# Performance work log

Hardware: AMD Instinct MI355X
Metric: run time of the kernel (lower is better)

Reference implementation:

```python
import jax, jax.numpy as jnp
import numpy as np
import math

N = 100000
E = 1600000
D_IN = 128
H = 128
OUT = 10
NEG = -1e30


def setup_inputs() -> dict:
    key = jax.random.key(0)
    ks = jax.random.split(key, 24)
    def lin(k, fi, fo):
        s = 1.0 / np.sqrt(fi)
        return jax.random.uniform(k, (fi, fo), jnp.float32, -s, s)
    inp = {
        'x': jax.random.normal(ks[0], (N, D_IN), jnp.float32),
        'edge_index': jax.random.randint(ks[1], (2, E), 0, N, jnp.int64),
        'W1': lin(ks[2], D_IN, H), 'b1': jnp.zeros((H,), jnp.float32),
        'ws1': lin(ks[3], H, 1), 'bs1': jnp.zeros((1,), jnp.float32),
        'W2': lin(ks[4], H, H), 'b2': jnp.zeros((H,), jnp.float32),
        'ws2': lin(ks[5], H, 1), 'bs2': jnp.zeros((1,), jnp.float32),
        'W3': lin(ks[6], H, H), 'b3': jnp.zeros((H,), jnp.float32),
        'ws3': lin(ks[7], H, 1), 'bs3': jnp.zeros((1,), jnp.float32),
        'M1': lin(ks[8], 2 * H, H), 'bm1': jnp.zeros((H,), jnp.float32),
        'M2': lin(ks[9], H, H // 2), 'bm2': jnp.zeros((H // 2,), jnp.float32),
        'M3': lin(ks[10], H // 2, OUT), 'bm3': jnp.zeros((OUT,), jnp.float32),
    }
    return inp


def _gcn(x, W, b, src, dst, node_mask, edge_mask):
    # GCNConv with self-loops: deg[i] = self_loop + in_degree over valid edges
    deg = node_mask + jax.ops.segment_sum(edge_mask, dst, num_segments=N)
    dinv = jnp.where(deg > 0, jax.lax.rsqrt(deg), 0.0)
    coef = edge_mask * dinv[src] * dinv[dst]            # [E]
    agg = jax.ops.segment_sum(coef[:, None] * x[src], dst, num_segments=N)
    agg = agg + (node_mask * dinv * dinv)[:, None] * x   # self-loop term
    return (agg @ W + b) * node_mask[:, None]


def _sag_pool(x, ws, bs, src, dst, node_mask, edge_mask, k):
    # score via 1-dim GCNConv, top-k (ratio 0.5) select, tanh gating, edge filtering
    score = _gcn(x, ws, bs, src, dst, node_mask, edge_mask)[:, 0]
    _, idx = jax.lax.top_k(jnp.where(node_mask > 0, score, -jnp.inf), k)
    new_mask = jnp.zeros((N,), x.dtype).at[idx].set(1.0)
    x_new = x * jnp.tanh(score)[:, None] * new_mask[:, None]
    e_new = edge_mask * new_mask[src] * new_mask[dst]
    return x_new, new_mask, e_new


def _readout(x, mask, k):
    mean = jnp.sum(x * mask[:, None], axis=0) / k
    mx = jnp.max(jnp.where(mask[:, None] > 0, x, NEG), axis=0)
    return jnp.concatenate([mean, mx])[None, :]   # [1, 2H]


def reference(x, edge_index, W1, b1, ws1, bs1, W2, b2, ws2, bs2, W3, b3, ws3, bs3, M1, bm1, M2, bm2, M3, bm3):
    src, dst = edge_index[0], edge_index[1]
    nm0 = jnp.ones((N,), jnp.float32)
    em0 = jnp.ones((E,), jnp.float32)
    k1 = math.ceil(0.5 * N)
    k2 = math.ceil(0.5 * k1)
    k3 = math.ceil(0.5 * k2)

    h1 = jax.nn.relu(_gcn(x, W1, b1, src, dst, nm0, em0))
    x1, nm1, em1 = _sag_pool(h1, ws1, bs1, src, dst, nm0, em0, k1)
    r1 = _readout(x1, nm1, k1)

    h2 = jax.nn.relu(_gcn(x1, W2, b2, src, dst, nm1, em1))
    x2, nm2, em2 = _sag_pool(h2, ws2, bs2, src, dst, nm1, em1, k2)
    r2 = _readout(x2, nm2, k2)

    h3 = jax.nn.relu(_gcn(x2, W3, b3, src, dst, nm2, em2))
    x3, nm3, em3 = _sag_pool(h3, ws3, bs3, src, dst, nm2, em2, k3)
    r3 = _readout(x3, nm3, k3)

    readout = r1 + r2 + r3                              # [1, 2H]
    y = jax.nn.relu(readout @ M1 + bm1)
    y = jax.nn.relu(y @ M2 + bm2)
    y = y @ M3 + bm3
    return jax.nn.log_softmax(y, axis=1)
```

## Files before the change

### kernel.cpp

```cpp
#include <hip/hip_runtime.h>
#include <cstdint>
#include <cstddef>

#define NN 100000
#define EE 1600000
#define HH 128
#define NB_N 391
#define NBKT 391
#define CAP 5120


static __device__ __forceinline__ unsigned fsort_(float f){
  unsigned u = __float_as_uint(f);
  return (u & 0x80000000u) ? ~u : (u | 0x80000000u);
}
static __device__ __forceinline__ unsigned bfbits_(float f){
  unsigned u = __float_as_uint(f);
  return (u + 0x7FFFu + ((u >> 16) & 1u)) >> 16;
}
static __device__ __forceinline__ unsigned bfpack_(float f0, float f1){
  return bfbits_(f0) | (bfbits_(f1) << 16);
}
static __device__ __forceinline__ float bflo_(unsigned u){ return __uint_as_float(u << 16); }
static __device__ __forceinline__ float bfhi_(unsigned u){ return __uint_as_float(u & 0xFFFF0000u); }

__global__ void k_edgeflag(const int* __restrict__ ei, unsigned* __restrict__ state,
                           unsigned* __restrict__ bktcnt){
  int t = threadIdx.x;
  if(t < 64){
    int v = ei[2*t + 1];
    unsigned long long m = __ballot(v != 0);
    if(t == 0) state[8] = (m == 0ull) ? 1u : 0u;
  }
  if(t >= 12 && t < 24) state[t] = 0u;
  for(int j=t; j<NBKT; j+=256) bktcnt[j] = 0u;
}

__global__ __launch_bounds__(256) void k_binA(const int* __restrict__ ei,
                     const unsigned* __restrict__ state,
                     unsigned* __restrict__ bktcnt, unsigned* __restrict__ staging){
  __shared__ unsigned lcnt[NBKT];
  __shared__ unsigned lloc[NBKT];
  int t = threadIdx.x;
  for(int j=t; j<NBKT; j+=256){ lcnt[j] = 0u; lloc[j] = 0u; }
  bool i64 = (state[8] != 0u);
  int e0 = blockIdx.x*4096;
  int es[16], ed[16];
  #pragma unroll
  for(int k=0;k<16;k++){
    int e = e0 + k*256 + t;
    int s = -1, d = 0;
    if(e < EE){
      if(i64){ s = ei[2*e]; d = ei[2*EE + 2*e]; }
      else   { s = ei[e];   d = ei[EE + e]; }
    }
    es[k] = s; ed[k] = d;
  }
  __syncthreads();
  #pragma unroll
  for(int k=0;k<16;k++){
    if(es[k] >= 0) atomicAdd(&lcnt[ed[k]>>8], 1u);
  }
  __syncthreads();
  for(int j=t; j<NBKT; j+=256){
    unsigned c = lcnt[j];
    lcnt[j] = c ? atomicAdd(&bktcnt[j], c) : 0u;
  }
  __syncthreads();
  #pragma unroll
  for(int k=0;k<16;k++){
    if(es[k] >= 0){
      int b = ed[k] >> 8;
      unsigned off = lcnt[b] + atomicAdd(&lloc[b], 1u);
      if(off < CAP)
        staging[(unsigned)b*CAP + off] = (unsigned)es[k] | (((unsigned)(ed[k] & 255)) << 17);
    }
  }
}

__global__ __launch_bounds__(256) void k_binB(const unsigned* __restrict__ staging,
                     const unsigned* __restrict__ bktcnt,
                     int* __restrict__ rs, int* __restrict__ rl, int* __restrict__ col,
                     float* __restrict__ dinv){
  __shared__ unsigned hist[256];
  __shared__ unsigned pref[256];
  __shared__ unsigned lfill[256];
  __shared__ unsigned baseSh;
  int t = threadIdx.x;
  int b = blockIdx.x;
  unsigned s = 0;
  for(int j=t; j<b; j+=256) s += bktcnt[j];
  pref[t] = s;
  __syncthreads();
  for(int off=128; off>0; off>>=1){
    if(t < off) pref[t] += pref[t+off];
    __syncthreads();
  }
  if(t == 0) baseSh = pref[0];
  __syncthreads();
  unsigned base = baseSh;
  unsigned cnt = bktcnt[b]; if(cnt > CAP) cnt = CAP;
  hist[t] = 0u; lfill[t] = 0u;
  __syncthreads();
  const unsigned* st = staging + (unsigned)b*CAP;
  for(unsigned i=t; i<cnt; i+=256) atomicAdd(&hist[st[i]>>17], 1u);
  __syncthreads();
  unsigned h = hist[t];
  pref[t] = h;
  __syncthreads();
  for(int off=1; off<256; off<<=1){
    unsigned u = (t >= off) ? pref[t-off] : 0u;
    __syncthreads();
    pref[t] += u;
    __syncthreads();
  }
  unsigned excl = pref[t] - h;
  int node = b*256 + t;
  if(node < NN){
    rs[node] = (int)(base + excl);
    rl[node] = (int)h;
    dinv[node] = rsqrtf(1.f + (float)h);
  }
  __syncthreads();
  pref[t] = excl;
  __syncthreads();
  for(unsigned i=t; i<cnt; i+=256){
    unsigned w = st[i];
    unsigned dl = w >> 17;
    unsigned pos = base + pref[dl] + atomicAdd(&lfill[dl], 1u);
    col[pos] = (int)(w & 0x1FFFFu);
  }
}

template<int MODE>
__global__ __launch_bounds__(256) void k_gemm(const void* __restrict__ xin_,
        const float* __restrict__ gate, const int* __restrict__ alist, int nrows,
        const float* __restrict__ W, unsigned short* __restrict__ y16){
  __shared__ float sX[16][68];
  __shared__ float sW[16][64];
  __shared__ int rowid[64];
  __shared__ float rowg[64];
  int row0 = blockIdx.x*64, col0 = blockIdx.y*64;
  int t = threadIdx.x;
  if(t < 64){
    int gr = row0 + t;
    int node = -1; float gg = 0.f;
    if(gr < nrows){
      node = MODE ? alist[gr] : gr;
      gg = MODE ? gate[node] : 1.f;
    }
    rowid[t] = node; rowg[t] = gg;
  }
  __syncthreads();
  int tx = t & 15, ty = t >> 4;
  float acc[4][4] = {{0.f}};
  const float* xf = (const float*)xin_;
  const unsigned short* xh = (const unsigned short*)xin_;
  for(int kb=0; kb<HH; kb+=16){
    #pragma unroll
    for(int j=0;j<4;j++){
      int r = (t>>4) + j*16;
      int k = t & 15;
      int node = rowid[r];
      float v = 0.f;
      if(node >= 0){
        if(MODE) v = __uint_as_float(((unsigned)xh[(size_t)node*HH + kb + k]) << 16) * rowg[r];
        else     v = xf[(size_t)node*HH + kb + k];
      }
      sX[k][r] = v;
    }
    #pragma unroll
    for(int j=0;j<4;j++){
      int k = (t>>6) + j*4;
      int c = t & 63;
      sW[k][c] = W[(size_t)(kb+k)*HH + col0 + c];
    }
    __syncthreads();
    #pragma unroll
    for(int k=0;k<16;k++){
      float4 xv = *(const float4*)&sX[k][ty*4];
      float4 wv = *(const float4*)&sW[k][tx*4];
      float xs[4] = {xv.x, xv.y, xv.z, xv.w};
      float wsv[4] = {wv.x, wv.y, wv.z, wv.w};
      #pragma unroll
      for(int a=0;a<4;a++)
        #pragma unroll
        for(int b=0;b<4;b++)
          acc[a][b] += xs[a]*wsv[b];
    }
    __syncthreads();
  }
  #pragma unroll
  for(int a=0;a<4;a++){
    int node = rowid[ty*4 + a];
    if(node >= 0){
      uint2 o;
      o.x = bfpack_(acc[a][0], acc[a][1]);
      o.y = bfpack_(acc[a][2], acc[a][3]);
      *(uint2*)&y16[(size_t)node*HH + col0 + tx*4] = o;
    }
  }
}

template<int LIST>
__global__ __launch_bounds__(256) void k_agg(const unsigned short* __restrict__ y16,
        const float* __restrict__ dinv,
        const int* __restrict__ rs, const int* __restrict__ rl,
        const int* __restrict__ col, const int* __restrict__ alist,
        const float* __restrict__ bias, const float* __restrict__ wsc,
        unsigned short* __restrict__ h16, float* __restrict__ p,
        unsigned* __restrict__ hist){
  if(blockIdx.x < 512) hist[blockIdx.x*256 + threadIdx.x] = 0u;
  int w = (blockIdx.x*256 + threadIdx.x) >> 6;
  int lane = threadIdx.x & 63;
  int g = lane >> 4, c = lane & 15;
  int node = LIST ? alist[w] : w;
  float di = dinv[node];
  int e0 = rs[node], len = rl[node];
  float a0=0,a1=0,a2=0,a3=0,a4=0,a5=0,a6=0,a7=0;
  int i = g;
  for(; i + 4 < len; i += 8){
    int s0 = col[e0+i], s1 = col[e0+i+4];
    float d0 = dinv[s0], d1 = dinv[s1];
    uint4 v0 = ((const uint4*)(y16 + (size_t)s0*HH))[c];
    uint4 v1 = ((const uint4*)(y16 + (size_t)s1*HH))[c];
    a0 += d0*bflo_(v0.x) + d1*bflo_(v1.x);
    a1 += d0*bfhi_(v0.x) + d1*bfhi_(v1.x);
    a2 += d0*bflo_(v0.y) + d1*bflo_(v1.y);
    a3 += d0*bfhi_(v0.y) + d1*bfhi_(v1.y);
    a4 += d0*bflo_(v0.z) + d1*bflo_(v1.z);
    a5 += d0*bfhi_(v0.z) + d1*bfhi_(v1.z);
    a6 += d0*bflo_(v0.w) + d1*bflo_(v1.w);
    a7 += d0*bfhi_(v0.w) + d1*bfhi_(v1.w);
  }
  if(i < len){
    int s = col[e0+i];
    float ds = dinv[s];
    uint4 v = ((const uint4*)(y16 + (size_t)s*HH))[c];
    a0 += ds*bflo_(v.x); a1 += ds*bfhi_(v.x);
    a2 += ds*bflo_(v.y); a3 += ds*bfhi_(v.y);
    a4 += ds*bflo_(v.z); a5 += ds*bfhi_(v.z);
    a6 += ds*bflo_(v.w); a7 += ds*bfhi_(v.w);
  }
  a0 += __shfl_xor(a0,16,64); a0 += __shfl_xor(a0,32,64);
  a1 += __shfl_xor(a1,16,64); a1 += __shfl_xor(a1,32,64);
  a2 += __shfl_xor(a2,16,64); a2 += __shfl_xor(a2,32,64);
  a3 += __shfl_xor(a3,16,64); a3 += __shfl_xor(a3,32,64);
  a4 += __shfl_xor(a4,16,64); a4 += __shfl_xor(a4,32,64);
  a5 += __shfl_xor(a5,16,64); a5 += __shfl_xor(a5,32,64);
  a6 += __shfl_xor(a6,16,64); a6 += __shfl_xor(a6,32,64);
  a7 += __shfl_xor(a7,16,64); a7 += __shfl_xor(a7,32,64);
  uint4 sv = ((const uint4*)(y16 + (size_t)node*HH))[c];
  const float4* b4 = (const float4*)bias;
  float4 bb0 = b4[2*c], bb1 = b4[2*c+1];
  float d2 = di*di;
  float o0 = fmaxf(di*a0 + d2*bflo_(sv.x) + bb0.x, 0.f);
  float o1 = fmaxf(di*a1 + d2*bfhi_(sv.x) + bb0.y, 0.f);
  float o2 = fmaxf(di*a2 + d2*bflo_(sv.y) + bb0.z, 0.f);
  float o3 = fmaxf(di*a3 + d2*bfhi_(sv.y) + bb0.w, 0.f);
  float o4 = fmaxf(di*a4 + d2*bflo_(sv.z) + bb1.x, 0.f);
  float o5 = fmaxf(di*a5 + d2*bfhi_(sv.z) + bb1.y, 0.f);
  float o6 = fmaxf(di*a6 + d2*bflo_(sv.w) + bb1.z, 0.f);
  float o7 = fmaxf(di*a7 + d2*bfhi_(sv.w) + bb1.w, 0.f);
  if(g == 0){
    uint4 o;
    o.x = bfpack_(o0,o1); o.y = bfpack_(o2,o3);
    o.z = bfpack_(o4,o5); o.w = bfpack_(o6,o7);
    ((uint4*)(h16 + (size_t)node*HH))[c] = o;
  }
  const float4* w4 = (const float4*)wsc;
  float4 w0 = w4[2*c], w1 = w4[2*c+1];
  float pp = o0*w0.x + o1*w0.y + o2*w0.z + o3*w0.w
           + o4*w1.x + o5*w1.y + o6*w1.z + o7*w1.w;
  pp += __shfl_xor(pp, 1, 64);
  pp += __shfl_xor(pp, 2, 64);
  pp += __shfl_xor(pp, 4, 64);
  pp += __shfl_xor(pp, 8, 64);
  if(lane == 0) p[node] = pp;
}

template<int LIST>
__global__ void k_score(const float* __restrict__ p, const float* __restrict__ dinv,
                        const int* __restrict__ rs, const int* __restrict__ rl,
                        const int* __restrict__ col, const int* __restrict__ alist, int n,
                        const float* __restrict__ bs, float* __restrict__ score,
                        unsigned* __restrict__ key, unsigned* __restrict__ hist){
  int w = blockIdx.x*256 + threadIdx.x;
  if(w >= n) return;
  int i = LIST ? alist[w] : w;
  float di = dinv[i];
  float s = 0.f;
  int e0 = rs[i], len = rl[i];
  for(int e=e0; e<e0+len; e++){
    int cidx = col[e];
    s += dinv[cidx]*p[cidx];
  }
  float sc = di*s + di*di*p[i] + bs[0];
  score[i] = sc;
  unsigned kv = fsort_(sc);
  key[i] = kv;
  atomicAdd(&hist[kv>>16], 1u);
}

__global__ void k_hist_lo(const unsigned* __restrict__ key, const unsigned* __restrict__ state,
                          unsigned* __restrict__ histB){
  int i = blockIdx.x*256 + threadIdx.x;
  if(i < NN){
    unsigned kv = key[i];
    if((kv >> 16) == state[0]) atomicAdd(&histB[kv & 0xFFFFu], 1u);
  }
}
__global__ void k_pick(const unsigned* __restrict__ hist, unsigned* __restrict__ state,
                       int k_in, int mode){
  __shared__ unsigned csum[256];
  int t = threadIdx.x;
  const uint4* h4 = (const uint4*)(hist + t*256);
  unsigned s = 0;
  for(int j=0;j<64;j++){ uint4 v = h4[j]; s += v.x+v.y+v.z+v.w; }
  csum[t] = s;
  __syncthreads();
  for(int off=1; off<256; off<<=1){
    unsigned v = (t+off < 256) ? csum[t+off] : 0u;
    __syncthreads();
    csum[t] += v;
    __syncthreads();
  }
  unsigned k = (mode == 0) ? (unsigned)k_in : state[1];
  unsigned above = csum[t] - s;
  if(above < k && above + s >= k){
    unsigned run = above;
    for(int j=255; j>=0; j--){
      unsigned c = hist[t*256+j];
      if(run + c >= k){
        if(mode == 0){ state[0] = (unsigned)(t*256+j); state[1] = k - run; }
        else { state[2] = (state[0] << 16) | (unsigned)(t*256+j); state[3] = k - run; }
        break;
      }
      run += c;
    }
  }
}

__global__ __launch_bounds__(256) void k_maskCR(unsigned* __restrict__ key,
        const float* __restrict__ score, const unsigned* __restrict__ state,
        const unsigned short* __restrict__ h16,
        unsigned char* __restrict__ selm, float* __restrict__ gate,
        int* __restrict__ alist_out, unsigned* __restrict__ acounter,
        float* __restrict__ rpart, int slotbase){
  __shared__ int wcnt[4];
  __shared__ int priorSh;
  __shared__ int redi[256];
  __shared__ float gl[256];
  __shared__ unsigned char slf[256];
  __shared__ float4 red[256];
  __shared__ float out2[256];
  int t = threadIdx.x;
  int i = blockIdx.x*256 + t;
  unsigned T = state[2];
  int trem = (int)state[3];
  unsigned kv = (i < NN) ? key[i] : 0u;
  bool match = (kv == T);
  unsigned long long m = __ballot(match);
  int lane = t & 63, wid = t >> 6;
  if(lane == 0) wcnt[wid] = __popcll(m);
  if(t == 0) priorSh = 0;
  __syncthreads();
  int hasMatch = wcnt[0] | wcnt[1] | wcnt[2] | wcnt[3];
  int bbase = blockIdx.x*256;
  if(hasMatch){
    int cm = 0;
    for(int j = t*4; j < bbase; j += 1024){
      uint4 kk = *(const uint4*)&key[j];
      cm += (kk.x==T) + (kk.y==T) + (kk.z==T) + (kk.w==T);
    }
    redi[t] = cm;
    __syncthreads();
    for(int off=128; off>0; off>>=1){
      if(t < off) redi[t] += redi[t+off];
      __syncthreads();
    }
    if(t == 0) priorSh = redi[0];
    __syncthreads();
  }
  int pre = 0;
  for(int w=0; w<wid; w++) pre += wcnt[w];
  int lrank = __popcll(m & ((1ull << lane) - 1ull));
  int rank = priorSh + pre + lrank;
  bool sel = (kv > T) || (match && rank < trem);
  float gg = sel ? tanhf(score[i]) : 0.f;
  gl[t] = gg;
  slf[t] = sel ? 1 : 0;
  if(i < NN){
    selm[i] = sel ? 1 : 0;
    gate[i] = gg;
    if(!sel) key[i] = 0u;
  }
  unsigned long long sm = __ballot(sel);
  unsigned abase = 0;
  if(lane == 0) abase = atomicAdd(acounter, (unsigned)__popcll(sm));
  abase = (unsigned)__shfl((int)abase, 0, 64);
  if(sel) alist_out[abase + __popcll(sm & ((1ull << lane) - 1ull))] = i;
  __syncthreads();
  int ch = t & 15;
  int slot = t >> 4;
  float mm[8] = {0,0,0,0,0,0,0,0};
  float MM[8] = {-1e30f,-1e30f,-1e30f,-1e30f,-1e30f,-1e30f,-1e30f,-1e30f};
  for(int itr=0; itr<16; itr++){
    int nl = slot + itr*16;
    int node = bbase + nl;
    if(node < NN && slf[nl]){
      float g = gl[nl];
      uint4 v = ((const uint4*)(h16 + (size_t)node*HH))[ch];
      float x0 = g*bflo_(v.x), x1 = g*bfhi_(v.x);
      float x2 = g*bflo_(v.y), x3 = g*bfhi_(v.y);
      float x4 = g*bflo_(v.z), x5 = g*bfhi_(v.z);
      float x6 = g*bflo_(v.w), x7 = g*bfhi_(v.w);
      mm[0]+=x0; mm[1]+=x1; mm[2]+=x2; mm[3]+=x3;
      mm[4]+=x4; mm[5]+=x5; mm[6]+=x6; mm[7]+=x7;
      MM[0]=fmaxf(MM[0],x0); MM[1]=fmaxf(MM[1],x1); MM[2]=fmaxf(MM[2],x2); MM[3]=fmaxf(MM[3],x3);
      MM[4]=fmaxf(MM[4],x4); MM[5]=fmaxf(MM[5],x5); MM[6]=fmaxf(MM[6],x6); MM[7]=fmaxf(MM[7],x7);
    }
  }
  #pragma unroll
  for(int half=0; half<2; half++){
    red[t] = make_float4(mm[half*4+0],mm[half*4+1],mm[half*4+2],mm[half*4+3]);
    __syncthreads();
    if(t < 16){
      float4 sacc = red[t];
      for(int j=1;j<16;j++){
        float4 o = red[t + 16*j];
        sacc.x += o.x; sacc.y += o.y; sacc.z += o.z; sacc.w += o.w;
      }
      int d = t*8 + half*4;
      out2[d+0] = sacc.x; out2[d+1] = sacc.y; out2[d+2] = sacc.z; out2[d+3] = sacc.w;
    }
    __syncthreads();
    red[t] = make_float4(MM[half*4+0],MM[half*4+1],MM[half*4+2],MM[half*4+3]);
    __syncthreads();
    if(t < 16){
      float4 sacc = red[t];
      for(int j=1;j<16;j++){
        float4 o = red[t + 16*j];
        sacc.x = fmaxf(sacc.x,o.x); sacc.y = fmaxf(sacc.y,o.y);
        sacc.z = fmaxf(sacc.z,o.z); sacc.w = fmaxf(sacc.w,o.w);
      }
      int d = 128 + t*8 + half*4;
      out2[d+0] = sacc.x; out2[d+1] = sacc.y; out2[d+2] = sacc.z; out2[d+3] = sacc.w;
    }
    __syncthreads();
  }
  rpart[(size_t)(slotbase + blockIdx.x)*256 + t] = out2[t];
}

__global__ __launch_bounds__(256) void k_compact(const int* __restrict__ alist, int n,
        const unsigned char* __restrict__ selm,
        const int* __restrict__ rs_old, const int* __restrict__ rl_old,
        const int* __restrict__ col_old,
        int* __restrict__ rs_new, int* __restrict__ rl_new, int* __restrict__ col_new,
        float* __restrict__ dinv, unsigned* __restrict__ ecnt){
  __shared__ unsigned gcnt[16];
  __shared__ unsigned gbase[16];
  __shared__ unsigned blkbase;
  int t = threadIdx.x;
  int g = t >> 4, lane = t & 15;
  int gsh = ((t >> 4) & 3) * 16;
  int idx = blockIdx.x*16 + g;
  int node = -1, e0 = 0, len = 0;
  if(idx < n){ node = alist[idx]; e0 = rs_old[node]; len = rl_old[node]; }
  int cnt = 0;
  for(int i=lane; i<len; i+=16) cnt += selm[col_old[e0+i]];
  cnt += __shfl_xor(cnt,1,64); cnt += __shfl_xor(cnt,2,64);
  cnt += __shfl_xor(cnt,4,64); cnt += __shfl_xor(cnt,8,64);
  if(lane == 0) gcnt[g] = (node >= 0) ? (unsigned)cnt : 0u;
  __syncthreads();
  if(t == 0){
    unsigned s = 0;
    for(int j=0;j<16;j++){ gbase[j] = s; s += gcnt[j]; }
    blkbase = s ? atomicAdd(ecnt, s) : 0u;
  }
  __syncthreads();
  unsigned base = blkbase + gbase[g];
  if(node >= 0 && lane == 0){
    rs_new[node] = (int)base;
    rl_new[node] = cnt;
    dinv[node] = rsqrtf(1.f + (float)cnt);
  }
  int pos = (int)base;
  for(int i0=0; i0<len; i0+=16){
    int i = i0 + lane;
    bool keep = false; int s = 0;
    if(i < len){ s = col_old[e0+i]; keep = (selm[s] != 0); }
    unsigned long long b = __ballot(keep);
    unsigned gb = (unsigned)((b >> gsh) & 0xFFFFull);
    int rank = __popc(gb & ((1u << lane) - 1u));
    if(keep) col_new[pos + rank] = s;
    pos += __popc(gb);
  }
}

__global__ void k_mlp(const float* __restrict__ rpart,
                      const float* __restrict__ M1, const float* __restrict__ bm1,
                      const float* __restrict__ M2, const float* __restrict__ bm2,
                      const float* __restrict__ M3, const float* __restrict__ bm3,
                      float* __restrict__ out){
  __shared__ float R[256];
  __shared__ float y1[128];
  __shared__ float y2[64];
  __shared__ float y3[16];
  int t = threadIdx.x;
  const float kinv[3] = {1.f/50000.f, 1.f/25000.f, 1.f/12500.f};
  if(t < 128){
    float acc = 0.f;
    for(int l=0; l<3; l++){
      float s0=0.f,s1=0.f,s2=0.f,s3=0.f;
      int base = l*NB_N;
      int j = 0;
      for(; j+3 < NB_N; j += 4){
        s0 += rpart[(size_t)(base+j  )*256 + t];
        s1 += rpart[(size_t)(base+j+1)*256 + t];
        s2 += rpart[(size_t)(base+j+2)*256 + t];
        s3 += rpart[(size_t)(base+j+3)*256 + t];
      }
      for(; j < NB_N; j++) s0 += rpart[(size_t)(base+j)*256 + t];
      acc += ((s0+s1)+(s2+s3)) * kinv[l];
    }
    R[t] = acc;
  } else {
    float acc = 0.f;
    for(int l=0; l<3; l++){
      float m0=-1e30f,m1=-1e30f,m2=-1e30f,m3=-1e30f;
      int base = l*NB_N;
      int j = 0;
      for(; j+3 < NB_N; j += 4){
        m0 = fmaxf(m0, rpart[(size_t)(base+j  )*256 + t]);
        m1 = fmaxf(m1, rpart[(size_t)(base+j+1)*256 + t]);
        m2 = fmaxf(m2, rpart[(size_t)(base+j+2)*256 + t]);
        m3 = fmaxf(m3, rpart[(size_t)(base+j+3)*256 + t]);
      }
      for(; j < NB_N; j++) m0 = fmaxf(m0, rpart[(size_t)(base+j)*256 + t]);
      acc += fmaxf(fmaxf(m0,m1), fmaxf(m2,m3));
    }
    R[t] = acc;
  }
  __syncthreads();
  if(t < 128){
    float a = bm1[t];
    for(int d=0; d<256; d++) a += R[d]*M1[d*128+t];
    y1[t] = fmaxf(a, 0.f);
  }
  __syncthreads();
  if(t < 64){
    float a = bm2[t];
    for(int d=0; d<128; d++) a += y1[d]*M2[d*64+t];
    y2[t] = fmaxf(a, 0.f);
  }
  __syncthreads();
  if(t < 10){
    float a = bm3[t];
    for(int d=0; d<64; d++) a += y2[d]*M3[d*10+t];
    y3[t] = a;
  }
  __syncthreads();
  if(t == 0){
    float mx = -1e30f;
    for(int o=0;o<10;o++) mx = fmaxf(mx, y3[o]);
    float s = 0.f;
    for(int o=0;o<10;o++) s += expf(y3[o]-mx);
    float ls = logf(s);
    for(int o=0;o<10;o++) out[o] = y3[o] - mx - ls;
  }
}

extern "C" void kernel_launch(void* const* d_in, const int* in_sizes, int n_in,
                              void* d_out, int out_size, void* d_ws, size_t ws_size,
                              hipStream_t stream){
  (void)in_sizes; (void)n_in; (void)out_size; (void)ws_size;
  const float* x  = (const float*)d_in[0];
  const int*   ei = (const int*)d_in[1];
  const float* W[3]   = {(const float*)d_in[2],  (const float*)d_in[6],  (const float*)d_in[10]};
  const float* bb[3]  = {(const float*)d_in[3],  (const float*)d_in[7],  (const float*)d_in[11]};
  const float* wsc[3] = {(const float*)d_in[4],  (const float*)d_in[8],  (const float*)d_in[12]};
  const float* bsc[3] = {(const float*)d_in[5],  (const float*)d_in[9],  (const float*)d_in[13]};
  const float* M1  = (const float*)d_in[14];
  const float* bm1 = (const float*)d_in[15];
  const float* M2  = (const float*)d_in[16];
  const float* bm2 = (const float*)d_in[17];
  const float* M3  = (const float*)d_in[18];
  const float* bm3 = (const float*)d_in[19];
  float* out = (float*)d_out;

  char* base = (char*)d_ws;
  size_t off = 0;
  auto alloc = [&](size_t bytes)->char*{
    char* ptr = base + off;
    off += (bytes + 511) & ~(size_t)511;
    return ptr;
  };
  unsigned short* y16  = (unsigned short*)alloc((size_t)NN*HH*2);
  unsigned short* h16  = (unsigned short*)alloc((size_t)NN*HH*2);
  int*      col0      = (int*)     alloc((size_t)EE*4);
  int*      col1      = (int*)     alloc((size_t)EE*4);
  int*      col2      = (int*)     alloc((size_t)EE*4);
  unsigned* staging   = (unsigned*)alloc((size_t)NBKT*CAP*4);
  int*      rs0       = (int*)     alloc((size_t)NN*4);
  int*      rl0       = (int*)     alloc((size_t)NN*4);
  int*      rs1       = (int*)     alloc((size_t)NN*4);
  int*      rl1       = (int*)     alloc((size_t)NN*4);
  int*      rs2       = (int*)     alloc((size_t)NN*4);
  int*      rl2       = (int*)     alloc((size_t)NN*4);
  float*    dinv      = (float*)   alloc((size_t)NN*4);
  float*    pbuf      = (float*)   alloc((size_t)NN*4);
  float*    score     = (float*)   alloc((size_t)NN*4);
  float*    gate      = (float*)   alloc((size_t)NN*4);
  unsigned* key       = (unsigned*)alloc((size_t)NN*4);
  unsigned char* selm = (unsigned char*)alloc((size_t)NN);
  int*      alistA    = (int*)     alloc((size_t)50000*4);
  int*      alistB    = (int*)     alloc((size_t)25000*4);
  unsigned* hist      = (unsigned*)alloc((size_t)2*65536*4);
  unsigned* bktcnt    = (unsigned*)alloc((size_t)(NBKT+1)*4);
  unsigned* state     = (unsigned*)alloc(256);
  float*    rpart     = (float*)   alloc((size_t)3*NB_N*256*4);

  k_edgeflag<<<1,256,0,stream>>>(ei, state, bktcnt);
  k_binA<<<NBKT,256,0,stream>>>(ei, state, bktcnt, staging);
  k_binB<<<NBKT,256,0,stream>>>(staging, bktcnt, rs0, rl0, col0, dinv);

  k_gemm<0><<<dim3(1563,2),256,0,stream>>>(x, nullptr, nullptr, NN, W[0], y16);
  k_agg<0><<<25000,256,0,stream>>>(y16, dinv, rs0, rl0, col0, nullptr, bb[0], wsc[0], h16, pbuf, hist);
  k_score<0><<<NB_N,256,0,stream>>>(pbuf, dinv, rs0, rl0, col0, nullptr, NN, bsc[0], score, key, hist);
  k_pick<<<1,256,0,stream>>>(hist, state, 50000, 0);
  k_hist_lo<<<NB_N,256,0,stream>>>(key, state, hist + 65536);
  k_pick<<<1,256,0,stream>>>(hist + 65536, state, 0, 1);
  k_maskCR<<<NB_N,256,0,stream>>>(key, score, state, h16, selm, gate, alistA, state+12, rpart, 0);
  k_compact<<<3125,256,0,stream>>>(alistA, 50000, selm, rs0, rl0, col0, rs1, rl1, col1, dinv, state+16);

  k_gemm<1><<<dim3(782,2),256,0,stream>>>(h16, gate, alistA, 50000, W[1], y16);
  k_agg<1><<<12500,256,0,stream>>>(y16, dinv, rs1, rl1, col1, alistA, bb[1], wsc[1], h16, pbuf, hist);
  k_score<1><<<196,256,0,stream>>>(pbuf, dinv, rs1, rl1, col1, alistA, 50000, bsc[1], score, key, hist);
  k_pick<<<1,256,0,stream>>>(hist, state, 25000, 0);
  k_hist_lo<<<NB_N,256,0,stream>>>(key, state, hist + 65536);
  k_pick<<<1,256,0,stream>>>(hist + 65536, state, 0, 1);
  k_maskCR<<<NB_N,256,0,stream>>>(key, score, state, h16, selm, gate, alistB, state+13, rpart, NB_N);
  k_compact<<<1563,256,0,stream>>>(alistB, 25000, selm, rs1, rl1, col1, rs2, rl2, col2, dinv, state+17);

  k_gemm<1><<<dim3(391,2),256,0,stream>>>(h16, gate, alistB, 25000, W[2], y16);
  k_agg<1><<<6250,256,0,stream>>>(y16, dinv, rs2, rl2, col2, alistB, bb[2], wsc[2], h16, pbuf, hist);
  k_score<1><<<98,256,0,stream>>>(pbuf, dinv, rs2, rl2, col2, alistB, 25000, bsc[2], score, key, hist);
  k_pick<<<1,256,0,stream>>>(hist, state, 12500, 0);
  k_hist_lo<<<NB_N,256,0,stream>>>(key, state, hist + 65536);
  k_pick<<<1,256,0,stream>>>(hist + 65536, state, 0, 1);
  k_maskCR<<<NB_N,256,0,stream>>>(key, score, state, h16, selm, gate, alistA, state+14, rpart, 2*NB_N);

  k_mlp<<<1,256,0,stream>>>(rpart, M1, bm1, M2, bm2, M3, bm3, out);
}
```

Before: 802.9 us.

## Fuse CSR build and top-k select stages into persistent kernels with grid barriers

Merges the edge-flag, bin-A and bin-B CSR construction kernels into one persistent 256-block kernel separated by software grid barriers. It also fuses the pick, low-histogram, mask/readout and edge-compaction kernels of each pooling stage into a single k_select kernel, with every block redundantly computing the histogram pick. The aim is to cut many small kernel launches and their serialization gaps. In exchange it depends on all 256 blocks being co-resident for the spin barrier, and the fused phases run with fewer blocks than the separate kernels did.

```diff
diff --git a/kernel.cpp b/kernel.cpp
--- a/kernel.cpp
+++ b/kernel.cpp
@@ -8,6 +8,7 @@
 #define NB_N 391
 #define NBKT 391
 #define CAP 5120
+#define GSEL 256
 
 
 static __device__ __forceinline__ unsigned fsort_(float f){
@@ -24,111 +25,159 @@
 static __device__ __forceinline__ float bflo_(unsigned u){ return __uint_as_float(u << 16); }
 static __device__ __forceinline__ float bfhi_(unsigned u){ return __uint_as_float(u & 0xFFFF0000u); }
 
-__global__ void k_edgeflag(const int* __restrict__ ei, unsigned* __restrict__ state,
-                           unsigned* __restrict__ bktcnt){
+static __device__ __forceinline__ void gridbar(unsigned* bar, unsigned nblk){
+  __syncthreads();
+  if(threadIdx.x == 0){
+    __threadfence();
+    unsigned g = __hip_atomic_load(&bar[1], __ATOMIC_RELAXED, __HIP_MEMORY_SCOPE_AGENT);
+    unsigned old = __hip_atomic_fetch_add(&bar[0], 1u, __ATOMIC_ACQ_REL, __HIP_MEMORY_SCOPE_AGENT);
+    if(old == nblk - 1u){
+      __hip_atomic_store(&bar[0], 0u, __ATOMIC_RELAXED, __HIP_MEMORY_SCOPE_AGENT);
+      __hip_atomic_store(&bar[1], g + 1u, __ATOMIC_RELEASE, __HIP_MEMORY_SCOPE_AGENT);
+    } else {
+      unsigned cur;
+      do {
+        __builtin_amdgcn_s_sleep(2);
+        cur = __hip_atomic_load(&bar[1], __ATOMIC_ACQUIRE, __HIP_MEMORY_SCOPE_AGENT);
+      } while(cur == g);
+    }
+    __threadfence();
+  }
+  __syncthreads();
+}
+
+static __device__ void pick_blk(const unsigned* __restrict__ hist, unsigned k,
+                                unsigned* csum, unsigned* outB, unsigned* outR){
+  __syncthreads();
   int t = threadIdx.x;
+  const uint4* h4 = (const uint4*)(hist + t*256);
+  unsigned s = 0;
+  for(int j=0;j<64;j++){ uint4 v = h4[j]; s += v.x+v.y+v.z+v.w; }
+  csum[t] = s;
+  __syncthreads();
+  for(int off=1; off<256; off<<=1){
+    unsigned v = (t+off < 256) ? csum[t+off] : 0u;
+    __syncthreads();
+    csum[t] += v;
+    __syncthreads();
+  }
+  unsigned above = csum[t] - s;
+  if(above < k && above + s >= k){
+    unsigned run = above;
+    for(int j=255; j>=0; j--){
+      unsigned c = hist[t*256+j];
+      if(run + c >= k){ *outB = (unsigned)(t*256+j); *outR = k - run; break; }
+      run += c;
+    }
+  }
+  __syncthreads();
+}
+
+__global__ __launch_bounds__(256) void k_csr(const int* __restrict__ ei,
+        unsigned* __restrict__ bktcnt, unsigned* __restrict__ staging,
+        int* __restrict__ rs, int* __restrict__ rl, int* __restrict__ col,
+        float* __restrict__ dinv, unsigned* __restrict__ state, unsigned* __restrict__ bar){
+  __shared__ unsigned lcnt[NBKT];
+  __shared__ unsigned lloc[NBKT];
+  __shared__ unsigned histo[256];
+  __shared__ unsigned pref[256];
+  __shared__ unsigned lfill[256];
+  __shared__ unsigned baseSh;
+  __shared__ int i64f;
+  int t = threadIdx.x;
+  int b = blockIdx.x;
+  int G = gridDim.x;
+  for(int j = b*256 + t; j < NBKT; j += G*256) bktcnt[j] = 0u;
+  if(b == 0 && t >= 12 && t < 24) state[t] = 0u;
   if(t < 64){
     int v = ei[2*t + 1];
     unsigned long long m = __ballot(v != 0);
-    if(t == 0) state[8] = (m == 0ull) ? 1u : 0u;
-  }
-  if(t >= 12 && t < 24) state[t] = 0u;
-  for(int j=t; j<NBKT; j+=256) bktcnt[j] = 0u;
-}
-
-__global__ __launch_bounds__(256) void k_binA(const int* __restrict__ ei,
-                     const unsigned* __restrict__ state,
-                     unsigned* __restrict__ bktcnt, unsigned* __restrict__ staging){
-  __shared__ unsigned lcnt[NBKT];
-  __shared__ unsigned lloc[NBKT];
-  int t = threadIdx.x;
-  for(int j=t; j<NBKT; j+=256){ lcnt[j] = 0u; lloc[j] = 0u; }
-  bool i64 = (state[8] != 0u);
-  int e0 = blockIdx.x*4096;
-  int es[16], ed[16];
-  #pragma unroll
-  for(int k=0;k<16;k++){
-    int e = e0 + k*256 + t;
-    int s = -1, d = 0;
-    if(e < EE){
-      if(i64){ s = ei[2*e]; d = ei[2*EE + 2*e]; }
-      else   { s = ei[e];   d = ei[EE + e]; }
-    }
-    es[k] = s; ed[k] = d;
-  }
-  __syncthreads();
-  #pragma unroll
-  for(int k=0;k<16;k++){
-    if(es[k] >= 0) atomicAdd(&lcnt[ed[k]>>8], 1u);
-  }
-  __syncthreads();
-  for(int j=t; j<NBKT; j+=256){
-    unsigned c = lcnt[j];
-    lcnt[j] = c ? atomicAdd(&bktcnt[j], c) : 0u;
-  }
-  __syncthreads();
-  #pragma unroll
-  for(int k=0;k<16;k++){
-    if(es[k] >= 0){
-      int b = ed[k] >> 8;
-      unsigned off = lcnt[b] + atomicAdd(&lloc[b], 1u);
-      if(off < CAP)
-        staging[(unsigned)b*CAP + off] = (unsigned)es[k] | (((unsigned)(ed[k] & 255)) << 17);
-    }
-  }
-}
-
-__global__ __launch_bounds__(256) void k_binB(const unsigned* __restrict__ staging,
-                     const unsigned* __restrict__ bktcnt,
-                     int* __restrict__ rs, int* __restrict__ rl, int* __restrict__ col,
-                     float* __restrict__ dinv){
-  __shared__ unsigned hist[256];
-  __shared__ unsigned pref[256];
-  __shared__ unsigned lfill[256];
-  __shared__ unsigned baseSh;
-  int t = threadIdx.x;
-  int b = blockIdx.x;
-  unsigned s = 0;
-  for(int j=t; j<b; j+=256) s += bktcnt[j];
-  pref[t] = s;
-  __syncthreads();
-  for(int off=128; off>0; off>>=1){
-    if(t < off) pref[t] += pref[t+off];
-    __syncthreads();
-  }
-  if(t == 0) baseSh = pref[0];
-  __syncthreads();
-  unsigned base = baseSh;
-  unsigned cnt = bktcnt[b]; if(cnt > CAP) cnt = CAP;
-  hist[t] = 0u; lfill[t] = 0u;
-  __syncthreads();
-  const unsigned* st = staging + (unsigned)b*CAP;
-  for(unsigned i=t; i<cnt; i+=256) atomicAdd(&hist[st[i]>>17], 1u);
-  __syncthreads();
-  unsigned h = hist[t];
-  pref[t] = h;
-  __syncthreads();
-  for(int off=1; off<256; off<<=1){
-    unsigned u = (t >= off) ? pref[t-off] : 0u;
-    __syncthreads();
-    pref[t] += u;
-    __syncthreads();
-  }
-  unsigned excl = pref[t] - h;
-  int node = b*256 + t;
-  if(node < NN){
-    rs[node] = (int)(base + excl);
-    rl[node] = (int)h;
-    dinv[node] = rsqrtf(1.f + (float)h);
-  }
-  __syncthreads();
-  pref[t] = excl;
-  __syncthreads();
-  for(unsigned i=t; i<cnt; i+=256){
-    unsigned w = st[i];
-    unsigned dl = w >> 17;
-    unsigned pos = base + pref[dl] + atomicAdd(&lfill[dl], 1u);
-    col[pos] = (int)(w & 0x1FFFFu);
+    if(t == 0) i64f = (m == 0ull) ? 1 : 0;
+  }
+  __syncthreads();
+  bool i64 = (i64f != 0);
+  gridbar(bar, G);
+  for(int chunk = b; chunk < NBKT; chunk += G){
+    __syncthreads();
+    for(int j=t; j<NBKT; j+=256){ lcnt[j] = 0u; lloc[j] = 0u; }
+    int e0 = chunk*4096;
+    int es[16], ed[16];
+    #pragma unroll
+    for(int k=0;k<16;k++){
+      int e = e0 + k*256 + t;
+      int s = -1, d = 0;
+      if(e < EE){
+        if(i64){ s = ei[2*e]; d = ei[2*EE + 2*e]; }
+        else   { s = ei[e];   d = ei[EE + e]; }
+      }
+      es[k] = s; ed[k] = d;
+    }
+    __syncthreads();
+    #pragma unroll
+    for(int k=0;k<16;k++){
+      if(es[k] >= 0) atomicAdd(&lcnt[ed[k]>>8], 1u);
+    }
+    __syncthreads();
+    for(int j=t; j<NBKT; j+=256){
+      unsigned c = lcnt[j];
+      lcnt[j] = c ? atomicAdd(&bktcnt[j], c) : 0u;
+    }
+    __syncthreads();
+    #pragma unroll
+    for(int k=0;k<16;k++){
+      if(es[k] >= 0){
+        int bk = ed[k] >> 8;
+        unsigned off = lcnt[bk] + atomicAdd(&lloc[bk], 1u);
+        if(off < CAP)
+          staging[(unsigned)bk*CAP + off] = (unsigned)es[k] | (((unsigned)(ed[k] & 255)) << 17);
+      }
+    }
+  }
+  gridbar(bar, G);
+  for(int bk = b; bk < NBKT; bk += G){
+    __syncthreads();
+    unsigned s = 0;
+    for(int j=t; j<bk; j+=256) s += bktcnt[j];
+    pref[t] = s;
+    __syncthreads();
+    for(int off=128; off>0; off>>=1){
+      if(t < off) pref[t] += pref[t+off];
+      __syncthreads();
+    }
+    if(t == 0) baseSh = pref[0];
+    __syncthreads();
+    unsigned base = baseSh;
+    unsigned cnt = bktcnt[bk]; if(cnt > CAP) cnt = CAP;
+    histo[t] = 0u; lfill[t] = 0u;
+    __syncthreads();
+    const unsigned* st = staging + (unsigned)bk*CAP;
+    for(unsigned i=t; i<cnt; i+=256) atomicAdd(&histo[st[i]>>17], 1u);
+    __syncthreads();
+    unsigned h = histo[t];
+    pref[t] = h;
+    __syncthreads();
+    for(int off=1; off<256; off<<=1){
+      unsigned u = (t >= off) ? pref[t-off] : 0u;
+      __syncthreads();
+      pref[t] += u;
+      __syncthreads();
+    }
+    unsigned excl = pref[t] - h;
+    int node = bk*256 + t;
+    if(node < NN){
+      rs[node] = (int)(base + excl);
+      rl[node] = (int)h;
+      dinv[node] = rsqrtf(1.f + (float)h);
+    }
+    __syncthreads();
+    pref[t] = excl;
+    __syncthreads();
+    for(unsigned i=t; i<cnt; i+=256){
+      unsigned w = st[i];
+      unsigned dl = w >> 17;
+      unsigned pos = base + pref[dl] + atomicAdd(&lfill[dl], 1u);
+      col[pos] = (int)(w & 0x1FFFFu);
+    }
   }
 }
 
@@ -302,51 +351,20 @@
   atomicAdd(&hist[kv>>16], 1u);
 }
 
-__global__ void k_hist_lo(const unsigned* __restrict__ key, const unsigned* __restrict__ state,
-                          unsigned* __restrict__ histB){
-  int i = blockIdx.x*256 + threadIdx.x;
-  if(i < NN){
-    unsigned kv = key[i];
-    if((kv >> 16) == state[0]) atomicAdd(&histB[kv & 0xFFFFu], 1u);
-  }
-}
-__global__ void k_pick(const unsigned* __restrict__ hist, unsigned* __restrict__ state,
-                       int k_in, int mode){
-  __shared__ unsigned csum[256];
-  int t = threadIdx.x;
-  const uint4* h4 = (const uint4*)(hist + t*256);
-  unsigned s = 0;
-  for(int j=0;j<64;j++){ uint4 v = h4[j]; s += v.x+v.y+v.z+v.w; }
-  csum[t] = s;
-  __syncthreads();
-  for(int off=1; off<256; off<<=1){
-    unsigned v = (t+off < 256) ? csum[t+off] : 0u;
-    __syncthreads();
-    csum[t] += v;
-    __syncthreads();
-  }
-  unsigned k = (mode == 0) ? (unsigned)k_in : state[1];
-  unsigned above = csum[t] - s;
-  if(above < k && above + s >= k){
-    unsigned run = above;
-    for(int j=255; j>=0; j--){
-      unsigned c = hist[t*256+j];
-      if(run + c >= k){
-        if(mode == 0){ state[0] = (unsigned)(t*256+j); state[1] = k - run; }
-        else { state[2] = (state[0] << 16) | (unsigned)(t*256+j); state[3] = k - run; }
-        break;
-      }
-      run += c;
-    }
-  }
-}
-
-__global__ __launch_bounds__(256) void k_maskCR(unsigned* __restrict__ key,
-        const float* __restrict__ score, const unsigned* __restrict__ state,
+__global__ __launch_bounds__(256) void k_select(unsigned* __restrict__ key,
+        const float* __restrict__ score, unsigned* __restrict__ hist, int k_in,
         const unsigned short* __restrict__ h16,
         unsigned char* __restrict__ selm, float* __restrict__ gate,
         int* __restrict__ alist_out, unsigned* __restrict__ acounter,
-        float* __restrict__ rpart, int slotbase){
+        float* __restrict__ rpart, int slotbase,
+        const int* __restrict__ alist_in, int n_compact,
+        const int* __restrict__ rs_old, const int* __restrict__ rl_old,
+        const int* __restrict__ col_old,
+        int* __restrict__ rs_new, int* __restrict__ rl_new, int* __restrict__ col_new,
+        float* __restrict__ dinv, unsigned* __restrict__ ecnt, int do_compact,
+        unsigned* __restrict__ bar){
+  __shared__ unsigned csum[256];
+  __shared__ unsigned sB, sR, sB2, sR2;
   __shared__ int wcnt[4];
   __shared__ int priorSh;
   __shared__ int redi[256];
@@ -354,147 +372,158 @@
   __shared__ unsigned char slf[256];
   __shared__ float4 red[256];
   __shared__ float out2[256];
-  int t = threadIdx.x;
-  int i = blockIdx.x*256 + t;
-  unsigned T = state[2];
-  int trem = (int)state[3];
-  unsigned kv = (i < NN) ? key[i] : 0u;
-  bool match = (kv == T);
-  unsigned long long m = __ballot(match);
-  int lane = t & 63, wid = t >> 6;
-  if(lane == 0) wcnt[wid] = __popcll(m);
-  if(t == 0) priorSh = 0;
-  __syncthreads();
-  int hasMatch = wcnt[0] | wcnt[1] | wcnt[2] | wcnt[3];
-  int bbase = blockIdx.x*256;
-  if(hasMatch){
-    int cm = 0;
-    for(int j = t*4; j < bbase; j += 1024){
-      uint4 kk = *(const uint4*)&key[j];
-      cm += (kk.x==T) + (kk.y==T) + (kk.z==T) + (kk.w==T);
-    }
-    redi[t] = cm;
-    __syncthreads();
-    for(int off=128; off>0; off>>=1){
-      if(t < off) redi[t] += redi[t+off];
-      __syncthreads();
-    }
-    if(t == 0) priorSh = redi[0];
-    __syncthreads();
-  }
-  int pre = 0;
-  for(int w=0; w<wid; w++) pre += wcnt[w];
-  int lrank = __popcll(m & ((1ull << lane) - 1ull));
-  int rank = priorSh + pre + lrank;
-  bool sel = (kv > T) || (match && rank < trem);
-  float gg = sel ? tanhf(score[i]) : 0.f;
-  gl[t] = gg;
-  slf[t] = sel ? 1 : 0;
-  if(i < NN){
-    selm[i] = sel ? 1 : 0;
-    gate[i] = gg;
-    if(!sel) key[i] = 0u;
-  }
-  unsigned long long sm = __ballot(sel);
-  unsigned abase = 0;
-  if(lane == 0) abase = atomicAdd(acounter, (unsigned)__popcll(sm));
-  abase = (unsigned)__shfl((int)abase, 0, 64);
-  if(sel) alist_out[abase + __popcll(sm & ((1ull << lane) - 1ull))] = i;
-  __syncthreads();
-  int ch = t & 15;
-  int slot = t >> 4;
-  float mm[8] = {0,0,0,0,0,0,0,0};
-  float MM[8] = {-1e30f,-1e30f,-1e30f,-1e30f,-1e30f,-1e30f,-1e30f,-1e30f};
-  for(int itr=0; itr<16; itr++){
-    int nl = slot + itr*16;
-    int node = bbase + nl;
-    if(node < NN && slf[nl]){
-      float g = gl[nl];
-      uint4 v = ((const uint4*)(h16 + (size_t)node*HH))[ch];
-      float x0 = g*bflo_(v.x), x1 = g*bfhi_(v.x);
-      float x2 = g*bflo_(v.y), x3 = g*bfhi_(v.y);
-      float x4 = g*bflo_(v.z), x5 = g*bfhi_(v.z);
-      float x6 = g*bflo_(v.w), x7 = g*bfhi_(v.w);
-      mm[0]+=x0; mm[1]+=x1; mm[2]+=x2; mm[3]+=x3;
-      mm[4]+=x4; mm[5]+=x5; mm[6]+=x6; mm[7]+=x7;
-      MM[0]=fmaxf(MM[0],x0); MM[1]=fmaxf(MM[1],x1); MM[2]=fmaxf(MM[2],x2); MM[3]=fmaxf(MM[3],x3);
-      MM[4]=fmaxf(MM[4],x4); MM[5]=fmaxf(MM[5],x5); MM[6]=fmaxf(MM[6],x6); MM[7]=fmaxf(MM[7],x7);
-    }
-  }
-  #pragma unroll
-  for(int half=0; half<2; half++){
-    red[t] = make_float4(mm[half*4+0],mm[half*4+1],mm[half*4+2],mm[half*4+3]);
-    __syncthreads();
-    if(t < 16){
-      float4 sacc = red[t];
-      for(int j=1;j<16;j++){
-        float4 o = red[t + 16*j];
-        sacc.x += o.x; sacc.y += o.y; sacc.z += o.z; sacc.w += o.w;
-      }
-      int d = t*8 + half*4;
-      out2[d+0] = sacc.x; out2[d+1] = sacc.y; out2[d+2] = sacc.z; out2[d+3] = sacc.w;
-    }
-    __syncthreads();
-    red[t] = make_float4(MM[half*4+0],MM[half*4+1],MM[half*4+2],MM[half*4+3]);
-    __syncthreads();
-    if(t < 16){
-      float4 sacc = red[t];
-      for(int j=1;j<16;j++){
-        float4 o = red[t + 16*j];
-        sacc.x = fmaxf(sacc.x,o.x); sacc.y = fmaxf(sacc.y,o.y);
-        sacc.z = fmaxf(sacc.z,o.z); sacc.w = fmaxf(sacc.w,o.w);
-      }
-      int d = 128 + t*8 + half*4;
-      out2[d+0] = sacc.x; out2[d+1] = sacc.y; out2[d+2] = sacc.z; out2[d+3] = sacc.w;
-    }
-    __syncthreads();
-  }
-  rpart[(size_t)(slotbase + blockIdx.x)*256 + t] = out2[t];
-}
-
-__global__ __launch_bounds__(256) void k_compact(const int* __restrict__ alist, int n,
-        const unsigned char* __restrict__ selm,
-        const int* __restrict__ rs_old, const int* __restrict__ rl_old,
-        const int* __restrict__ col_old,
-        int* __restrict__ rs_new, int* __restrict__ rl_new, int* __restrict__ col_new,
-        float* __restrict__ dinv, unsigned* __restrict__ ecnt){
   __shared__ unsigned gcnt[16];
   __shared__ unsigned gbase[16];
   __shared__ unsigned blkbase;
   int t = threadIdx.x;
-  int g = t >> 4, lane = t & 15;
-  int gsh = ((t >> 4) & 3) * 16;
-  int idx = blockIdx.x*16 + g;
-  int node = -1, e0 = 0, len = 0;
-  if(idx < n){ node = alist[idx]; e0 = rs_old[node]; len = rl_old[node]; }
-  int cnt = 0;
-  for(int i=lane; i<len; i+=16) cnt += selm[col_old[e0+i]];
-  cnt += __shfl_xor(cnt,1,64); cnt += __shfl_xor(cnt,2,64);
-  cnt += __shfl_xor(cnt,4,64); cnt += __shfl_xor(cnt,8,64);
-  if(lane == 0) gcnt[g] = (node >= 0) ? (unsigned)cnt : 0u;
-  __syncthreads();
-  if(t == 0){
-    unsigned s = 0;
-    for(int j=0;j<16;j++){ gbase[j] = s; s += gcnt[j]; }
-    blkbase = s ? atomicAdd(ecnt, s) : 0u;
-  }
-  __syncthreads();
-  unsigned base = blkbase + gbase[g];
-  if(node >= 0 && lane == 0){
-    rs_new[node] = (int)base;
-    rl_new[node] = cnt;
-    dinv[node] = rsqrtf(1.f + (float)cnt);
-  }
-  int pos = (int)base;
-  for(int i0=0; i0<len; i0+=16){
-    int i = i0 + lane;
-    bool keep = false; int s = 0;
-    if(i < len){ s = col_old[e0+i]; keep = (selm[s] != 0); }
-    unsigned long long b = __ballot(keep);
-    unsigned gb = (unsigned)((b >> gsh) & 0xFFFFull);
-    int rank = __popc(gb & ((1u << lane) - 1u));
-    if(keep) col_new[pos + rank] = s;
-    pos += __popc(gb);
+  int G = gridDim.x;
+  unsigned* histB = hist + 65536;
+  pick_blk(hist, (unsigned)k_in, csum, &sB, &sR);
+  unsigned hi = sB, krem = sR;
+  for(int i = blockIdx.x*256 + t; i < NN; i += G*256){
+    unsigned kv = key[i];
+    if((kv >> 16) == hi) atomicAdd(&histB[kv & 0xFFFFu], 1u);
+  }
+  gridbar(bar, G);
+  pick_blk(histB, krem, csum, &sB2, &sR2);
+  unsigned T = (hi << 16) | sB2;
+  int trem = (int)sR2;
+  for(int chunk = blockIdx.x; chunk < NB_N; chunk += G){
+    __syncthreads();
+    int bbase = chunk*256;
+    int i = bbase + t;
+    unsigned kv = (i < NN) ? key[i] : 0u;
+    bool match = (kv == T);
+    unsigned long long m = __ballot(match);
+    int lane = t & 63, wid = t >> 6;
+    if(lane == 0) wcnt[wid] = __popcll(m);
+    if(t == 0) priorSh = 0;
+    __syncthreads();
+    int hasMatch = wcnt[0] | wcnt[1] | wcnt[2] | wcnt[3];
+    if(hasMatch){
+      int cm = 0;
+      for(int j = t*4; j < bbase; j += 1024){
+        uint4 kk = *(const uint4*)&key[j];
+        cm += (kk.x==T) + (kk.y==T) + (kk.z==T) + (kk.w==T);
+      }
+      redi[t] = cm;
+      __syncthreads();
+      for(int off=128; off>0; off>>=1){
+        if(t < off) redi[t] += redi[t+off];
+        __syncthreads();
+      }
+      if(t == 0) priorSh = redi[0];
+      __syncthreads();
+    }
+    int pre = 0;
+    for(int w=0; w<wid; w++) pre += wcnt[w];
+    int lrank = __popcll(m & ((1ull << lane) - 1ull));
+    int rank = priorSh + pre + lrank;
+    bool sel = (kv > T) || (match && rank < trem);
+    float gg = sel ? tanhf(score[i]) : 0.f;
+    gl[t] = gg;
+    slf[t] = sel ? 1 : 0;
+    if(i < NN){
+      selm[i] = sel ? 1 : 0;
+      gate[i] = gg;
+    }
+    unsigned long long sm = __ballot(sel);
+    unsigned abase = 0;
+    if(lane == 0) abase = atomicAdd(acounter, (unsigned)__popcll(sm));
+    abase = (unsigned)__shfl((int)abase, 0, 64);
+    if(sel) alist_out[abase + __popcll(sm & ((1ull << lane) - 1ull))] = i;
+    __syncthreads();
+    int ch = t & 15;
+    int slot = t >> 4;
+    float mm[8] = {0,0,0,0,0,0,0,0};
+    float MM[8] = {-1e30f,-1e30f,-1e30f,-1e30f,-1e30f,-1e30f,-1e30f,-1e30f};
+    for(int itr=0; itr<16; itr++){
+      int nl = slot + itr*16;
+      int node = bbase + nl;
+      if(node < NN && slf[nl]){
+        float g = gl[nl];
+        uint4 v = ((const uint4*)(h16 + (size_t)node*HH))[ch];
+        float x0 = g*bflo_(v.x), x1 = g*bfhi_(v.x);
+        float x2 = g*bflo_(v.y), x3 = g*bfhi_(v.y);
+        float x4 = g*bflo_(v.z), x5 = g*bfhi_(v.z);
+        float x6 = g*bflo_(v.w), x7 = g*bfhi_(v.w);
+        mm[0]+=x0; mm[1]+=x1; mm[2]+=x2; mm[3]+=x3;
+        mm[4]+=x4; mm[5]+=x5; mm[6]+=x6; mm[7]+=x7;
+        MM[0]=fmaxf(MM[0],x0); MM[1]=fmaxf(MM[1],x1); MM[2]=fmaxf(MM[2],x2); MM[3]=fmaxf(MM[3],x3);
+        MM[4]=fmaxf(MM[4],x4); MM[5]=fmaxf(MM[5],x5); MM[6]=fmaxf(MM[6],x6); MM[7]=fmaxf(MM[7],x7);
+      }
+    }
+    #pragma unroll
+    for(int half=0; half<2; half++){
+      red[t] = make_float4(mm[half*4+0],mm[half*4+1],mm[half*4+2],mm[half*4+3]);
+      __syncthreads();
+      if(t < 16){
+        float4 sacc = red[t];
+        for(int j=1;j<16;j++){
+          float4 o = red[t + 16*j];
+          sacc.x += o.x; sacc.y += o.y; sacc.z += o.z; sacc.w += o.w;
+        }
+        int d = t*8 + half*4;
+        out2[d+0] = sacc.x; out2[d+1] = sacc.y; out2[d+2] = sacc.z; out2[d+3] = sacc.w;
+      }
+      __syncthreads();
+      red[t] = make_float4(MM[half*4+0],MM[half*4+1],MM[half*4+2],MM[half*4+3]);
+      __syncthreads();
+      if(t < 16){
+        float4 sacc = red[t];
+        for(int j=1;j<16;j++){
+          float4 o = red[t + 16*j];
+          sacc.x = fmaxf(sacc.x,o.x); sacc.y = fmaxf(sacc.y,o.y);
+          sacc.z = fmaxf(sacc.z,o.z); sacc.w = fmaxf(sacc.w,o.w);
+        }
+        int d = 128 + t*8 + half*4;
+        out2[d+0] = sacc.x; out2[d+1] = sacc.y; out2[d+2] = sacc.z; out2[d+3] = sacc.w;
+      }
+      __syncthreads();
+    }
+    rpart[(size_t)(slotbase + chunk)*256 + t] = out2[t];
+  }
+  gridbar(bar, G);
+  if(do_compact){
+    for(int i = blockIdx.x*256 + t; i < NN; i += G*256)
+      if(!selm[i]) key[i] = 0u;
+    int g = t >> 4, lane = t & 15;
+    int gsh = ((t >> 4) & 3) * 16;
+    for(int gidx = blockIdx.x*16; gidx < n_compact; gidx += G*16){
+      __syncthreads();
+      int idx = gidx + g;
+      int node = -1, e0 = 0, len = 0;
+      if(idx < n_compact){ node = alist_in[idx]; e0 = rs_old[node]; len = rl_old[node]; }
+      int cnt = 0;
+      for(int i=lane; i<len; i+=16) cnt += selm[col_old[e0+i]];
+      cnt += __shfl_xor(cnt,1,64); cnt += __shfl_xor(cnt,2,64);
+      cnt += __shfl_xor(cnt,4,64); cnt += __shfl_xor(cnt,8,64);
+      if(lane == 0) gcnt[g] = (node >= 0) ? (unsigned)cnt : 0u;
+      __syncthreads();
+      if(t == 0){
+        unsigned s = 0;
+        for(int j=0;j<16;j++){ gbase[j] = s; s += gcnt[j]; }
+        blkbase = s ? atomicAdd(ecnt, s) : 0u;
+      }
+      __syncthreads();
+      unsigned base = blkbase + gbase[g];
+      if(node >= 0 && lane == 0){
+        rs_new[node] = (int)base;
+        rl_new[node] = cnt;
+        dinv[node] = rsqrtf(1.f + (float)cnt);
+      }
+      int pos = (int)base;
+      for(int i0=0; i0<len; i0+=16){
+        int i = i0 + lane;
+        bool keep = false; int s = 0;
+        if(i < len){ s = col_old[e0+i]; keep = (selm[s] != 0); }
+        unsigned long long bmask = __ballot(keep);
+        unsigned gb = (unsigned)((bmask >> gsh) & 0xFFFFull);
+        int rank = __popc(gb & ((1u << lane) - 1u));
+        if(keep) col_new[pos + rank] = s;
+        pos += __popc(gb);
+      }
+    }
   }
 }
 
@@ -619,37 +648,44 @@
   unsigned* hist      = (unsigned*)alloc((size_t)2*65536*4);
   unsigned* bktcnt    = (unsigned*)alloc((size_t)(NBKT+1)*4);
   unsigned* state     = (unsigned*)alloc(256);
+  unsigned* bar       = (unsigned*)alloc(256);
   float*    rpart     = (float*)   alloc((size_t)3*NB_N*256*4);
 
-  k_edgeflag<<<1,256,0,stream>>>(ei, state, bktcnt);
-  k_binA<<<NBKT,256,0,stream>>>(ei, state, bktcnt, staging);
-  k_binB<<<NBKT,256,0,stream>>>(staging, bktcnt, rs0, rl0, col0, dinv);
+  hipMemsetAsync(bar, 0, 64, stream);
+
+  k_csr<<<GSEL,256,0,stream>>>(ei, bktcnt, staging, rs0, rl0, col0, dinv, state, bar);
+
+  int kk[3] = {50000, 25000, 12500};
+  int ncmp[3] = {50000, 25000, 0};
+  int docmp[3] = {1, 1, 0};
+  int slotb[3] = {0, NB_N, 2*NB_N};
+  int* aout[3] = {alistA, alistB, alistA};
+  int* ain[3]  = {alistA, alistB, alistB};
+  unsigned* acnt[3] = {state+12, state+13, state+14};
+  unsigned* ecnt[3] = {state+16, state+17, state+17};
+  int* rsO[3] = {rs0, rs1, rs2}; int* rlO[3] = {rl0, rl1, rl2}; int* colO[3] = {col0, col1, col2};
+  int* rsN[3] = {rs1, rs2, rs2}; int* rlN[3] = {rl1, rl2, rl2}; int* colN[3] = {col1, col2, col2};
 
   k_gemm<0><<<dim3(1563,2),256,0,stream>>>(x, nullptr, nullptr, NN, W[0], y16);
   k_agg<0><<<25000,256,0,stream>>>(y16, dinv, rs0, rl0, col0, nullptr, bb[0], wsc[0], h16, pbuf, hist);
   k_score<0><<<NB_N,256,0,stream>>>(pbuf, dinv, rs0, rl0, col0, nullptr, NN, bsc[0], score, key, hist);
-  k_pick<<<1,256,0,stream>>>(hist, state, 50000, 0);
-  k_hist_lo<<<NB_N,256,0,stream>>>(key, state, hist + 65536);
-  k_pick<<<1,256,0,stream>>>(hist + 65536, state, 0, 1);
-  k_maskCR<<<NB_N,256,0,stream>>>(key, score, state, h16, selm, gate, alistA, state+12, rpart, 0);
-  k_compact<<<3125,256,0,stream>>>(alistA, 50000, selm, rs0, rl0, col0, rs1, rl1, col1, dinv, state+16);
+  k_select<<<GSEL,256,0,stream>>>(key, score, hist, kk[0], h16, selm, gate, aout[0], acnt[0],
+                                  rpart, slotb[0], ain[0], ncmp[0], rsO[0], rlO[0], colO[0],
+                                  rsN[0], rlN[0], colN[0], dinv, ecnt[0], docmp[0], bar);
 
   k_gemm<1><<<dim3(782,2),256,0,stream>>>(h16, gate, alistA, 50000, W[1], y16);
   k_agg<1><<<12500,256,0,stream>>>(y16, dinv, rs1, rl1, col1, alistA, bb[1], wsc[1], h16, pbuf, hist);
   k_score<1><<<196,256,0,stream>>>(pbuf, dinv, rs1, rl1, col1, alistA, 50000, bsc[1], score, key, hist);
-  k_pick<<<1,256,0,stream>>>(hist, state, 25000, 0);
-  k_hist_lo<<<NB_N,256,0,stream>>>(key, state, hist + 65536);
-  k_pick<<<1,256,0,stream>>>(hist + 65536, state, 0, 1);
-  k_maskCR<<<NB_N,256,0,stream>>>(key, score, state, h16, selm, gate, alistB, state+13, rpart, NB_N);
-  k_compact<<<1563,256,0,stream>>>(alistB, 25000, selm, rs1, rl1, col1, rs2, rl2, col2, dinv, state+17);
+  k_select<<<GSEL,256,0,stream>>>(key, score, hist, kk[1], h16, selm, gate, aout[1], acnt[1],
+                                  rpart, slotb[1], ain[1], ncmp[1], rsO[1], rlO[1], colO[1],
+                                  rsN[1], rlN[1], colN[1], dinv, ecnt[1], docmp[1], bar);
 
   k_gemm<1><<<dim3(391,2),256,0,stream>>>(h16, gate, alistB, 25000, W[2], y16);
   k_agg<1><<<6250,256,0,stream>>>(y16, dinv, rs2, rl2, col2, alistB, bb[2], wsc[2], h16, pbuf, hist);
   k_score<1><<<98,256,0,stream>>>(pbuf, dinv, rs2, rl2, col2, alistB, 25000, bsc[2], score, key, hist);
-  k_pick<<<1,256,0,stream>>>(hist, state, 12500, 0);
-  k_hist_lo<<<NB_N,256,0,stream>>>(key, state, hist + 65536);
-  k_pick<<<1,256,0,stream>>>(hist + 65536, state, 0, 1);
-  k_maskCR<<<NB_N,256,0,stream>>>(key, score, state, h16, selm, gate, alistA, state+14, rpart, 2*NB_N);
+  k_select<<<GSEL,256,0,stream>>>(key, score, hist, kk[2], h16, selm, gate, aout[2], acnt[2],
+                                  rpart, slotb[2], ain[2], ncmp[2], rsO[2], rlO[2], colO[2],
+                                  rsN[2], rlN[2], colN[2], dinv, ecnt[2], docmp[2], bar);
 
   k_mlp<<<1,256,0,stream>>>(rpart, M1, bm1, M2, bm2, M3, bm3, out);
 }
```

Result: slower. 1.205 ms (+50.1%).
